# Kernel tuning notes

Measured on AMD Instinct MI355X. Metric: run time of the kernel, lower is better.

The kernel has to match this reference:

```python
import jax, jax.numpy as jnp
import numpy as np

N, V_DIM, P_DIM, Q_DIM, C_DIM, H_DIM = 1536, 128, 16, 16, 16, 32
N_MOL, N_EDGE, LAYERS = 64, 16384, 3
TAU, GAMMA = 0.2, 1.0


def setup_inputs() -> dict:
    key = jax.random.key(0)
    ks = jax.random.split(key, 16)
    rng = np.random.default_rng(0)

    v_features = jax.random.normal(ks[0], (N, V_DIM), dtype=jnp.float32)

    # molecule -> node assignment: 64 molecules x 24 nodes each (block structure)
    mol_id = np.repeat(np.arange(N_MOL), N // N_MOL)
    mnm = np.zeros((N_MOL, N), dtype=np.float32)
    mnm[mol_id, np.arange(N)] = 1.0
    mol_node_mask = (mnm - 1.0) * 1e9  # 0 where assigned, -1e9 otherwise

    # node-edge incidence matrix [N, E]
    src = rng.integers(0, N, N_EDGE)
    dst = rng.integers(0, N, N_EDGE)
    nem = np.zeros((N, N_EDGE), dtype=np.float32)
    nem[src, np.arange(N_EDGE)] = 1.0
    nem[dst, np.arange(N_EDGE)] = 1.0
    node_edge_mask = np.zeros((N, N_EDGE), dtype=np.float32)

    def lin(k, fan_in, fan_out):
        kw, kb = jax.random.split(k)
        s = 1.0 / np.sqrt(fan_in)
        W = jax.random.uniform(kw, (fan_in, fan_out), jnp.float32, -s, s)
        b = jax.random.uniform(kb, (fan_out,), jnp.float32, -s, s)
        return W, b

    Wp, bp = lin(ks[1], V_DIM, P_DIM)
    Wq, bq = lin(ks[2], V_DIM, Q_DIM)
    Wc, bc = lin(ks[3], Q_DIM, C_DIM)
    W1, b1 = lin(ks[4], P_DIM + Q_DIM + C_DIM, H_DIM)
    Wdp, bdp = lin(ks[5], H_DIM, P_DIM)
    Wdq, bdq = lin(ks[6], H_DIM, Q_DIM)
    Wa, ba = lin(ks[7], P_DIM + Q_DIM, 1)

    return dict(v_features=v_features,
                mol_node_matrix=jnp.asarray(mnm), mol_node_mask=jnp.asarray(mol_node_mask),
                node_edge_matrix=jnp.asarray(nem), node_edge_mask=jnp.asarray(node_edge_mask),
                Wp=Wp, bp=bp, Wq=Wq, bq=bq, Wc=Wc, bc=bc,
                W1=W1, b1=b1, Wdp=Wdp, bdp=bdp, Wdq=Wdq, bdq=bdq, Wa=Wa, ba=ba)


def _safe_pair_norm(q):
    # pairwise ||q_i - q_j|| with grad-safe sqrt (zero diag)
    sq = ((q[None, :, :] - q[:, None, :]) ** 2).sum(-1)  # [N,N]
    return jnp.where(sq > 0, jnp.sqrt(jnp.where(sq > 0, sq, 1.0)), 0.0)


def reference(v_features, mol_node_matrix, mol_node_mask, node_edge_matrix, node_edge_mask,
              Wp, bp, Wq, bq, Wc, bc, W1, b1, Wdp, bdp, Wdq, bdq, Wa, ba):
    n = v_features.shape[0]
    m = mol_node_matrix.T @ mol_node_matrix                      # [N,N] same-molecule mask
    e = node_edge_matrix @ node_edge_matrix.T                    # [N,N] adjacency counts
    e = e * (1.0 - jnp.eye(n, dtype=e.dtype))                    # zero diagonal

    p = v_features @ Wp + bp                                     # [N,p]
    q = v_features @ Wq + bq                                     # [N,q]
    c_loss = jnp.linalg.norm(mol_node_matrix @ q)

    for _ in range(LAYERS):
        diff = q[None, :, :] - q[:, None, :]                     # [N,N,q]
        cenc = diff @ Wc + bc                                    # [N,N,c]  (large intermediate, as in torch)
        c = jnp.einsum('ij,ijc->ic', m, cenc)                    # masked sum over j
        h = jax.nn.relu(jnp.concatenate([p, q, c], axis=1) @ W1 + b1)
        dp = jnp.tanh(h @ Wdp + bdp)
        dq = jnp.tanh(h @ Wdq + bdq)
        p = p + TAU * dp
        q = q + TAU * dq
        c_loss = c_loss + jnp.linalg.norm(mol_node_matrix @ q)

    x = jnp.concatenate([p, q], axis=1)                          # [N, p+q]
    w = (x @ Wa + ba)[:, 0]                                      # [N]
    att = jax.nn.softmax(mol_node_matrix * w[None, :] + mol_node_mask, axis=1)  # [n_mol, N]
    f = att @ x                                                  # [n_mol, p+q]

    s_loss = jnp.abs(p).sum()
    a_loss = (e * jax.nn.relu(_safe_pair_norm(q) - GAMMA)).sum()
    return (f, s_loss, c_loss, a_loss)
```

## Files before the change

### kernel.cpp

```cpp
#include <hip/hip_runtime.h>
#include <hip/hip_bf16.h>
#include <math.h>

#define N_NODES 1536
#define V_DIMC  128
#define NMOL    64
#define NEDGE   16384
#define MAXM    24
#define SCANB   2048
#define TAU     0.2f

__device__ __forceinline__ float ldv(const void* p, int i, bool b16) {
    if (b16) {
        unsigned int u = ((unsigned int)((const unsigned short*)p)[i]) << 16;
        float f; __builtin_memcpy(&f, &u, 4); return f;
    }
    return ((const float*)p)[i];
}
__device__ __forceinline__ void stv(void* p, int i, float v, bool b16) {
    if (b16) ((__hip_bfloat16*)p)[i] = __float2bfloat16(v);
    else     ((float*)p)[i] = v;
}
__device__ __forceinline__ bool is_b16(const void* mnm) {
    return (*(const unsigned int*)mnm) != 0x3F800000u;
}

__global__ __launch_bounds__(384) void k_mega(
        const void* __restrict__ mnm, const void* __restrict__ nem,
        const void* __restrict__ v,
        const void* __restrict__ Wp, const void* __restrict__ bp,
        const void* __restrict__ Wq, const void* __restrict__ bq,
        const void* __restrict__ Wc, const void* __restrict__ bc,
        const void* __restrict__ W1, const void* __restrict__ b1,
        const void* __restrict__ Wdp, const void* __restrict__ bdp,
        const void* __restrict__ Wdq, const void* __restrict__ bdq,
        const void* __restrict__ Wa, const void* __restrict__ ba,
        unsigned int* __restrict__ srowA, unsigned int* __restrict__ srowB,
        float* __restrict__ qg, float* __restrict__ s_part,
        float* __restrict__ c_part, void* __restrict__ out) {
    __shared__ __align__(16) float R1[4096];
    __shared__ __align__(16) float R2[24 * 132];
    __shared__ float red[512];
    __shared__ int   mi[MAXM];
    __shared__ float mw[MAXM];
    __shared__ float msum[16], wv[MAXM], attw[MAXM];
    __shared__ int   nmem_s;
    __shared__ float rs_s, inv_s;

    const int t = threadIdx.x;
    const bool b16 = is_b16(mnm);

    if (blockIdx.x >= NMOL) {
        int sb = blockIdx.x - NMOL;
        const int stride = SCANB * 384;
        if (b16) {
            const int total8 = N_NODES * NEDGE / 8;
            const uint4* src = (const uint4*)nem;
            for (int i = sb * 384 + t; i < total8; i += stride) {
                uint4 x = src[i];
                if ((x.x | x.y | x.z | x.w) == 0u) continue;
                int base = i * 8, row = base >> 14, k0 = base & (NEDGE - 1);
                unsigned int wd[4] = {x.x, x.y, x.z, x.w};
                for (int w2 = 0; w2 < 4; ++w2) {
                    unsigned int ww = wd[w2];
                    if (!ww) continue;
                    if (ww & 0xFFFFu) { int k = k0 + 2 * w2;
                        atomicMin(&srowA[k], (unsigned)row); atomicMin(&srowB[k], ~(unsigned)row); }
                    if (ww >> 16)     { int k = k0 + 2 * w2 + 1;
                        atomicMin(&srowA[k], (unsigned)row); atomicMin(&srowB[k], ~(unsigned)row); }
                }
            }
        } else {
            const int total4 = N_NODES * NEDGE / 4;
            const float4* src = (const float4*)nem;
            for (int i = sb * 384 + t; i < total4; i += stride) {
                float4 x = src[i];
                if (x.x == 0.f && x.y == 0.f && x.z == 0.f && x.w == 0.f) continue;
                int base = i * 4, row = base >> 14, k0 = base & (NEDGE - 1);
                float vv[4] = {x.x, x.y, x.z, x.w};
                for (int u = 0; u < 4; ++u) if (vv[u] != 0.f) {
                    int k = k0 + u;
                    atomicMin(&srowA[k], (unsigned)row); atomicMin(&srowB[k], ~(unsigned)row);
                }
            }
        }
        return;
    }

    const int g = blockIdx.x;
    const int m = t >> 4, d = t & 15;

    if (t == 0) nmem_s = 0;
    if (t < MAXM) { mi[t] = 0; mw[t] = 0.f; }
    __syncthreads();

    if (!b16) {
        const float4* wp4 = (const float4*)Wp; const float4* wq4 = (const float4*)Wq;
        float4* r14 = (float4*)R1;
        for (int i = t; i < 512; i += 384) { r14[i] = wp4[i]; r14[512 + i] = wq4[i]; }
    } else {
        for (int i = t; i < 2048; i += 384) { R1[i] = ldv(Wp, i, true); R1[2048 + i] = ldv(Wq, i, true); }
    }
    for (int j = t; j < N_NODES; j += 384) {
        float w = ldv(mnm, g * N_NODES + j, b16);
        if (w != 0.f) {
            int pos = atomicAdd(&nmem_s, 1);
            if (pos < MAXM) { mi[pos] = j; mw[pos] = w; }
        }
    }
    __syncthreads();
    const int nm = (nmem_s > MAXM) ? MAXM : nmem_s;

    if (!b16) {
        for (int idx = t; idx < 24 * 32; idx += 384) {
            int row = idx >> 5, col = idx & 31;
            float4 x = ((const float4*)v)[mi[row] * 32 + col];
            *((float4*)&R2[row * 132 + col * 4]) = x;
        }
    } else {
        for (int idx = t; idx < 24 * 128; idx += 384) {
            int row = idx >> 7, e = idx & 127;
            R2[row * 132 + e] = ldv(v, mi[row] * V_DIMC + e, true);
        }
    }
    if (t == 0) { float s = 0.f; for (int m2 = 0; m2 < nm; ++m2) s += mw[m2]; rs_s = s; }
    __syncthreads();
    const float rs = rs_s;

    float accp = ldv(bp, d, b16), accq = ldv(bq, d, b16);
    {
        const float* vr = &R2[m * 132];
#pragma unroll 8
        for (int e = 0; e < V_DIMC; ++e) {
            float vv = vr[e];
            accp += vv * R1[e * 16 + d];
            accq += vv * R1[2048 + e * 16 + d];
        }
    }
    __syncthreads();

    float* P  = &R2[0];     float* Q  = &R2[408];
    float* XQ = &R2[816];   float* XC = &R2[1224];
    float* H  = &R2[1632];
    P[m * 17 + d] = accp;  Q[m * 17 + d] = accq;
    for (int i = t; i < 1536; i += 384) R1[i] = ldv(W1, i, b16);
    for (int i = t; i < 512; i += 384) { R1[1536 + i] = ldv(Wdp, i, b16); R1[2048 + i] = ldv(Wdq, i, b16); }
    if (t < 256) R1[2560 + t] = ldv(Wc, t, b16);
    if (t < 16) { R1[2816 + t] = ldv(bc, t, b16); R1[2864 + t] = ldv(bdp, t, b16); R1[2880 + t] = ldv(bdq, t, b16); }
    if (t < 32) { R1[2832 + t] = ldv(b1, t, b16); R1[2896 + t] = ldv(Wa, t, b16); }
    if (t == 0) R1[2928] = ldv(ba, 0, b16);

    for (int layer = 0; layer < 4; ++layer) {
        __syncthreads();
        if (t < 16) {
            float s = 0.f;
            for (int m2 = 0; m2 < nm; ++m2) s += mw[m2] * Q[m2 * 17 + t];
            msum[t] = s;
        }
        __syncthreads();
        if (t == 0) {
            float ss = 0.f;
            for (int e = 0; e < 16; ++e) ss += msum[e] * msum[e];
            c_part[layer * NMOL + g] = ss;
        }
        if (layer == 3) break;
        float pi = 0.f, qi = 0.f;
        if (m < nm) {
            pi = P[m * 17 + d]; qi = Q[m * 17 + d];
            XQ[m * 17 + d] = mw[m] * (msum[d] - rs * qi);
        }
        __syncthreads();
        if (m < nm) {
            float c = mw[m] * rs * R1[2816 + d];
            for (int e = 0; e < 16; ++e) c += XQ[m * 17 + e] * R1[2560 + e * 16 + d];
            XC[m * 17 + d] = c;
        }
        __syncthreads();
        if (m < nm) {
            float h0 = R1[2832 + d], h1 = R1[2832 + 16 + d];
            for (int e = 0; e < 48; ++e) {
                float xv = (e < 16) ? P[m * 17 + e] : (e < 32) ? Q[m * 17 + e - 16] : XC[m * 17 + e - 32];
                h0 += xv * R1[e * 32 + d];
                h1 += xv * R1[e * 32 + 16 + d];
            }
            H[m * 33 + d] = fmaxf(h0, 0.f); H[m * 33 + 16 + d] = fmaxf(h1, 0.f);
        }
        __syncthreads();
        if (m < nm) {
            float dp = R1[2864 + d], dq = R1[2880 + d];
            for (int e = 0; e < 32; ++e) {
                float hv = H[m * 33 + e];
                dp += hv * R1[1536 + e * 16 + d];
                dq += hv * R1[2048 + e * 16 + d];
            }
            P[m * 17 + d] = pi + TAU * tanhf(dp);
            Q[m * 17 + d] = qi + TAU * tanhf(dq);
        }
    }
    __syncthreads();

    if (m < nm) qg[mi[m] * 16 + d] = Q[m * 17 + d];

    red[t] = (m < nm) ? fabsf(P[m * 17 + d]) : 0.f;
    if (t < 128) red[384 + t] = 0.f;
    __syncthreads();
    for (int s = 256; s > 0; s >>= 1) { if (t < s) red[t] += red[t + s]; __syncthreads(); }
    if (t == 0) s_part[g] = red[0];

    if (t < nm) {
        float acc = R1[2928];
        for (int e = 0; e < 16; ++e)
            acc += P[t * 17 + e] * R1[2896 + e] + Q[t * 17 + e] * R1[2896 + 16 + e];
        wv[t] = mw[t] * acc;
    }
    __syncthreads();
    if (t == 0) {
        float mx = -3.0e38f;
        for (int m2 = 0; m2 < nm; ++m2) mx = fmaxf(mx, wv[m2]);
        float s = 0.f;
        for (int m2 = 0; m2 < nm; ++m2) { float ex = expf(wv[m2] - mx); attw[m2] = ex; s += ex; }
        inv_s = 1.f / s;
    }
    __syncthreads();
    if (t < 32) {
        float acc = 0.f;
        for (int m2 = 0; m2 < nm; ++m2)
            acc += attw[m2] * ((t < 16) ? P[m2 * 17 + t] : Q[m2 * 17 + t - 16]);
        stv(out, g * 32 + t, acc * inv_s, b16);
    }
}

__global__ __launch_bounds__(1024) void DynamicGraphEncoder_85985245266279_kernel(
        const void* __restrict__ mnm,
        const unsigned int* __restrict__ srowA, const unsigned int* __restrict__ srowB,
        const float* __restrict__ qg, const float* __restrict__ s_part,
        const float* __restrict__ c_part, void* __restrict__ out) {
    __shared__ float red[1024];
    const int t = threadIdx.x;
    const bool b16 = is_b16(mnm);

    float local = 0.f;
    for (int k = t; k < NEDGE; k += 1024) {
        unsigned int a = srowA[k], b = ~srowB[k];
        if (a < b && b < (unsigned)N_NODES) {
            const float4* qa = (const float4*)(qg + a * 16);
            const float4* qb = (const float4*)(qg + b * 16);
            float d2 = 0.f;
#pragma unroll
            for (int c4 = 0; c4 < 4; ++c4) {
                float4 xa = qa[c4], xb = qb[c4];
                float dx = xa.x - xb.x, dy = xa.y - xb.y, dz = xa.z - xb.z, dw = xa.w - xb.w;
                d2 += dx * dx + dy * dy + dz * dz + dw * dw;
            }
            if (d2 > 0.f) {
                float r = sqrtf(d2) - 1.0f;
                if (r > 0.f) local += 2.f * r;
            }
        }
    }
    red[t] = local; __syncthreads();
    for (int s = 512; s > 0; s >>= 1) { if (t < s) red[t] += red[t + s]; __syncthreads(); }
    float a_loss = red[0]; __syncthreads();

    red[t] = (t < NMOL) ? s_part[t] : 0.f; __syncthreads();
    for (int s = 512; s > 0; s >>= 1) { if (t < s) red[t] += red[t + s]; __syncthreads(); }
    float s_loss = red[0]; __syncthreads();

    float cl[4];
    for (int stg = 0; stg < 4; ++stg) {
        red[t] = (t < NMOL) ? c_part[stg * NMOL + t] : 0.f; __syncthreads();
        for (int s = 512; s > 0; s >>= 1) { if (t < s) red[t] += red[t + s]; __syncthreads(); }
        cl[stg] = red[0]; __syncthreads();
    }
    if (t == 0) {
        stv(out, 2048, s_loss, b16);
        stv(out, 2049, sqrtf(cl[0]) + sqrtf(cl[1]) + sqrtf(cl[2]) + sqrtf(cl[3]), b16);
        stv(out, 2050, a_loss, b16);
    }
}

extern "C" void kernel_launch(void* const* d_in, const int* in_sizes, int n_in,
                              void* d_out, int out_size, void* d_ws, size_t ws_size,
                              hipStream_t stream) {
    const void* v    = d_in[0];
    const void* mnm  = d_in[1];
    const void* nem  = d_in[3];
    const void* Wp  = d_in[5];  const void* bp  = d_in[6];
    const void* Wq  = d_in[7];  const void* bq  = d_in[8];
    const void* Wc  = d_in[9];  const void* bc  = d_in[10];
    const void* W1  = d_in[11]; const void* b1  = d_in[12];
    const void* Wdp = d_in[13]; const void* bdp = d_in[14];
    const void* Wdq = d_in[15]; const void* bdq = d_in[16];
    const void* Wa  = d_in[17]; const void* ba  = d_in[18];

    float*        ws     = (float*)d_ws;
    float*        qg     = ws;
    float*        s_part = qg + N_NODES * 16;
    float*        c_part = s_part + NMOL;
    unsigned int* srowA  = (unsigned int*)(c_part + 4 * NMOL);
    unsigned int* srowB  = srowA + NEDGE;

    hipMemsetAsync(srowA, 0xFF, 2 * NEDGE * sizeof(unsigned int), stream);

    k_mega<<<NMOL + SCANB, 384, 0, stream>>>(mnm, nem, v,
            Wp, bp, Wq, bq, Wc, bc, W1, b1, Wdp, bdp, Wdq, bdq, Wa, ba,
            srowA, srowB, qg, s_part, c_part, d_out);
    DynamicGraphEncoder_85985245266279_kernel<<<1, 1024, 0, stream>>>(
            mnm, srowA, srowB, qg, s_part, c_part, d_out);
}
```

Before: 290.2 us.

## Split a-loss into parallel kernel, shrink k_mega LDS, use wave-shuffle final reduce

Moves the per-edge a-loss computation out of the single-block final kernel into a 64-block kernel that writes partial sums. The final kernel becomes a single 64-thread wave that reduces the partials with shuffles instead of repeated 1024-wide shared-memory tree reductions. It also drops the Wp/Wq staging in LDS: those weights are read directly from global memory, and only the layer weights stay in a smaller shared buffer. The smaller LDS footprint could raise occupancy for the scan blocks, at the cost of more global loads in the projection loop and one extra kernel launch.

```diff
diff --git a/kernel.cpp b/kernel.cpp
--- a/kernel.cpp
+++ b/kernel.cpp
@@ -38,8 +38,8 @@
         unsigned int* __restrict__ srowA, unsigned int* __restrict__ srowB,
         float* __restrict__ qg, float* __restrict__ s_part,
         float* __restrict__ c_part, void* __restrict__ out) {
-    __shared__ __align__(16) float R1[4096];
     __shared__ __align__(16) float R2[24 * 132];
+    __shared__ float WL[2944];
     __shared__ float red[512];
     __shared__ int   mi[MAXM];
     __shared__ float mw[MAXM];
@@ -94,13 +94,6 @@
     if (t < MAXM) { mi[t] = 0; mw[t] = 0.f; }
     __syncthreads();
 
-    if (!b16) {
-        const float4* wp4 = (const float4*)Wp; const float4* wq4 = (const float4*)Wq;
-        float4* r14 = (float4*)R1;
-        for (int i = t; i < 512; i += 384) { r14[i] = wp4[i]; r14[512 + i] = wq4[i]; }
-    } else {
-        for (int i = t; i < 2048; i += 384) { R1[i] = ldv(Wp, i, true); R1[2048 + i] = ldv(Wq, i, true); }
-    }
     for (int j = t; j < N_NODES; j += 384) {
         float w = ldv(mnm, g * N_NODES + j, b16);
         if (w != 0.f) {
@@ -123,7 +116,15 @@
             R2[row * 132 + e] = ldv(v, mi[row] * V_DIMC + e, true);
         }
     }
-    if (t == 0) { float s = 0.f; for (int m2 = 0; m2 < nm; ++m2) s += mw[m2]; rs_s = s; }
+    for (int i = t; i < 1536; i += 384) WL[i] = ldv(W1, i, b16);
+    for (int i = t; i < 512; i += 384) { WL[1536 + i] = ldv(Wdp, i, b16); WL[2048 + i] = ldv(Wdq, i, b16); }
+    if (t < 256) WL[2560 + t] = ldv(Wc, t, b16);
+    if (t < 16) { WL[2816 + t] = ldv(bc, t, b16); WL[2864 + t] = ldv(bdp, t, b16); WL[2880 + t] = ldv(bdq, t, b16); }
+    if (t < 32) { WL[2832 + t] = ldv(b1, t, b16); WL[2896 + t] = ldv(Wa, t, b16); }
+    if (t == 0) {
+        WL[2928] = ldv(ba, 0, b16);
+        float s = 0.f; for (int m2 = 0; m2 < nm; ++m2) s += mw[m2]; rs_s = s;
+    }
     __syncthreads();
     const float rs = rs_s;
 
@@ -133,8 +134,8 @@
 #pragma unroll 8
         for (int e = 0; e < V_DIMC; ++e) {
             float vv = vr[e];
-            accp += vv * R1[e * 16 + d];
-            accq += vv * R1[2048 + e * 16 + d];
+            accp += vv * ldv(Wp, e * 16 + d, b16);
+            accq += vv * ldv(Wq, e * 16 + d, b16);
         }
     }
     __syncthreads();
@@ -143,12 +144,6 @@
     float* XQ = &R2[816];   float* XC = &R2[1224];
     float* H  = &R2[1632];
     P[m * 17 + d] = accp;  Q[m * 17 + d] = accq;
-    for (int i = t; i < 1536; i += 384) R1[i] = ldv(W1, i, b16);
-    for (int i = t; i < 512; i += 384) { R1[1536 + i] = ldv(Wdp, i, b16); R1[2048 + i] = ldv(Wdq, i, b16); }
-    if (t < 256) R1[2560 + t] = ldv(Wc, t, b16);
-    if (t < 16) { R1[2816 + t] = ldv(bc, t, b16); R1[2864 + t] = ldv(bdp, t, b16); R1[2880 + t] = ldv(bdq, t, b16); }
-    if (t < 32) { R1[2832 + t] = ldv(b1, t, b16); R1[2896 + t] = ldv(Wa, t, b16); }
-    if (t == 0) R1[2928] = ldv(ba, 0, b16);
 
     for (int layer = 0; layer < 4; ++layer) {
         __syncthreads();
@@ -171,27 +166,27 @@
         }
         __syncthreads();
         if (m < nm) {
-            float c = mw[m] * rs * R1[2816 + d];
-            for (int e = 0; e < 16; ++e) c += XQ[m * 17 + e] * R1[2560 + e * 16 + d];
+            float c = mw[m] * rs * WL[2816 + d];
+            for (int e = 0; e < 16; ++e) c += XQ[m * 17 + e] * WL[2560 + e * 16 + d];
             XC[m * 17 + d] = c;
         }
         __syncthreads();
         if (m < nm) {
-            float h0 = R1[2832 + d], h1 = R1[2832 + 16 + d];
+            float h0 = WL[2832 + d], h1 = WL[2832 + 16 + d];
             for (int e = 0; e < 48; ++e) {
                 float xv = (e < 16) ? P[m * 17 + e] : (e < 32) ? Q[m * 17 + e - 16] : XC[m * 17 + e - 32];
-                h0 += xv * R1[e * 32 + d];
-                h1 += xv * R1[e * 32 + 16 + d];
+                h0 += xv * WL[e * 32 + d];
+                h1 += xv * WL[e * 32 + 16 + d];
             }
             H[m * 33 + d] = fmaxf(h0, 0.f); H[m * 33 + 16 + d] = fmaxf(h1, 0.f);
         }
         __syncthreads();
         if (m < nm) {
-            float dp = R1[2864 + d], dq = R1[2880 + d];
+            float dp = WL[2864 + d], dq = WL[2880 + d];
             for (int e = 0; e < 32; ++e) {
                 float hv = H[m * 33 + e];
-                dp += hv * R1[1536 + e * 16 + d];
-                dq += hv * R1[2048 + e * 16 + d];
+                dp += hv * WL[1536 + e * 16 + d];
+                dq += hv * WL[2048 + e * 16 + d];
             }
             P[m * 17 + d] = pi + TAU * tanhf(dp);
             Q[m * 17 + d] = qi + TAU * tanhf(dq);
@@ -208,9 +203,9 @@
     if (t == 0) s_part[g] = red[0];
 
     if (t < nm) {
-        float acc = R1[2928];
+        float acc = WL[2928];
         for (int e = 0; e < 16; ++e)
-            acc += P[t * 17 + e] * R1[2896 + e] + Q[t * 17 + e] * R1[2896 + 16 + e];
+            acc += P[t * 17 + e] * WL[2896 + e] + Q[t * 17 + e] * WL[2896 + 16 + e];
         wv[t] = mw[t] * acc;
     }
     __syncthreads();
@@ -230,52 +225,52 @@
     }
 }
 
-__global__ __launch_bounds__(1024) void DynamicGraphEncoder_85985245266279_kernel(
+__global__ __launch_bounds__(256) void k_aloss(
+        const unsigned int* __restrict__ srowA, const unsigned int* __restrict__ srowB,
+        const float* __restrict__ qg, float* __restrict__ apart) {
+    __shared__ float red[256];
+    const int t = threadIdx.x;
+    const int k = blockIdx.x * 256 + t;
+    float local = 0.f;
+    unsigned int a = srowA[k], b = ~srowB[k];
+    if (a < b && b < (unsigned)N_NODES) {
+        const float4* qa = (const float4*)(qg + a * 16);
+        const float4* qb = (const float4*)(qg + b * 16);
+        float d2 = 0.f;
+#pragma unroll
+        for (int c4 = 0; c4 < 4; ++c4) {
+            float4 xa = qa[c4], xb = qb[c4];
+            float dx = xa.x - xb.x, dy = xa.y - xb.y, dz = xa.z - xb.z, dw = xa.w - xb.w;
+            d2 += dx * dx + dy * dy + dz * dz + dw * dw;
+        }
+        if (d2 > 0.f) {
+            float r = sqrtf(d2) - 1.0f;
+            if (r > 0.f) local = 2.f * r;
+        }
+    }
+    red[t] = local; __syncthreads();
+    for (int s = 128; s > 0; s >>= 1) { if (t < s) red[t] += red[t + s]; __syncthreads(); }
+    if (t == 0) apart[blockIdx.x] = red[0];
+}
+
+__global__ void DynamicGraphEncoder_85985245266279_kernel(
         const void* __restrict__ mnm,
-        const unsigned int* __restrict__ srowA, const unsigned int* __restrict__ srowB,
-        const float* __restrict__ qg, const float* __restrict__ s_part,
-        const float* __restrict__ c_part, void* __restrict__ out) {
-    __shared__ float red[1024];
-    const int t = threadIdx.x;
+        const float* __restrict__ s_part, const float* __restrict__ c_part,
+        const float* __restrict__ apart, void* __restrict__ out) {
     const bool b16 = is_b16(mnm);
-
-    float local = 0.f;
-    for (int k = t; k < NEDGE; k += 1024) {
-        unsigned int a = srowA[k], b = ~srowB[k];
-        if (a < b && b < (unsigned)N_NODES) {
-            const float4* qa = (const float4*)(qg + a * 16);
-            const float4* qb = (const float4*)(qg + b * 16);
-            float d2 = 0.f;
-#pragma unroll
-            for (int c4 = 0; c4 < 4; ++c4) {
-                float4 xa = qa[c4], xb = qb[c4];
-                float dx = xa.x - xb.x, dy = xa.y - xb.y, dz = xa.z - xb.z, dw = xa.w - xb.w;
-                d2 += dx * dx + dy * dy + dz * dz + dw * dw;
-            }
-            if (d2 > 0.f) {
-                float r = sqrtf(d2) - 1.0f;
-                if (r > 0.f) local += 2.f * r;
-            }
-        }
-    }
-    red[t] = local; __syncthreads();
-    for (int s = 512; s > 0; s >>= 1) { if (t < s) red[t] += red[t + s]; __syncthreads(); }
-    float a_loss = red[0]; __syncthreads();
-
-    red[t] = (t < NMOL) ? s_part[t] : 0.f; __syncthreads();
-    for (int s = 512; s > 0; s >>= 1) { if (t < s) red[t] += red[t + s]; __syncthreads(); }
-    float s_loss = red[0]; __syncthreads();
-
-    float cl[4];
-    for (int stg = 0; stg < 4; ++stg) {
-        red[t] = (t < NMOL) ? c_part[stg * NMOL + t] : 0.f; __syncthreads();
-        for (int s = 512; s > 0; s >>= 1) { if (t < s) red[t] += red[t + s]; __syncthreads(); }
-        cl[stg] = red[0]; __syncthreads();
+    int t = threadIdx.x;
+    float s  = s_part[t], a = apart[t];
+    float c0 = c_part[t],       c1 = c_part[64 + t];
+    float c2 = c_part[128 + t], c3 = c_part[192 + t];
+    for (int off = 32; off > 0; off >>= 1) {
+        s  += __shfl_down(s, off);   a  += __shfl_down(a, off);
+        c0 += __shfl_down(c0, off);  c1 += __shfl_down(c1, off);
+        c2 += __shfl_down(c2, off);  c3 += __shfl_down(c3, off);
     }
     if (t == 0) {
-        stv(out, 2048, s_loss, b16);
-        stv(out, 2049, sqrtf(cl[0]) + sqrtf(cl[1]) + sqrtf(cl[2]) + sqrtf(cl[3]), b16);
-        stv(out, 2050, a_loss, b16);
+        stv(out, 2048, s, b16);
+        stv(out, 2049, sqrtf(c0) + sqrtf(c1) + sqrtf(c2) + sqrtf(c3), b16);
+        stv(out, 2050, a, b16);
     }
 }
 
@@ -297,7 +292,8 @@
     float*        qg     = ws;
     float*        s_part = qg + N_NODES * 16;
     float*        c_part = s_part + NMOL;
-    unsigned int* srowA  = (unsigned int*)(c_part + 4 * NMOL);
+    float*        apart  = c_part + 4 * NMOL;
+    unsigned int* srowA  = (unsigned int*)(apart + NMOL);
     unsigned int* srowB  = srowA + NEDGE;
 
     hipMemsetAsync(srowA, 0xFF, 2 * NEDGE * sizeof(unsigned int), stream);
@@ -305,6 +301,7 @@
     k_mega<<<NMOL + SCANB, 384, 0, stream>>>(mnm, nem, v,
             Wp, bp, Wq, bq, Wc, bc, W1, b1, Wdp, bdp, Wdq, bdq, Wa, ba,
             srowA, srowB, qg, s_part, c_part, d_out);
-    DynamicGraphEncoder_85985245266279_kernel<<<1, 1024, 0, stream>>>(
-            mnm, srowA, srowB, qg, s_part, c_part, d_out);
-}
+    k_aloss<<<NEDGE / 256, 256, 0, stream>>>(srowA, srowB, qg, apart);
+    DynamicGraphEncoder_85985245266279_kernel<<<1, 64, 0, stream>>>(
+            mnm, s_part, c_part, apart, d_out);
+}
```

After: 243.8 us. 16.0% less time.
